# Performance work log

Measured on AMD Instinct MI355X. Metric: run time of the kernel, lower is better.

The kernel has to match this reference:

```python
import jax, jax.numpy as jnp
import numpy as np

N = 50000
E = 800000
IN_C = 128
HEADS = 2
HID = 64  # out_channels // heads (concat=True)
NEG_SLOPE = 0.2


def setup_inputs() -> dict:
    key = jax.random.key(0)
    ks = jax.random.split(key, 8)
    x = jax.random.normal(ks[0], (N, IN_C), dtype=jnp.float32)
    edge_index = jax.random.randint(ks[1], (2, E), 0, N, dtype=jnp.int64)
    edge_weight = jax.random.uniform(ks[2], (E,), dtype=jnp.float32)
    s = 1.0 / np.sqrt(IN_C)
    W_l = jax.random.normal(ks[3], (IN_C, HEADS * HID), dtype=jnp.float32) * s
    b_l = jnp.zeros((HEADS * HID,), dtype=jnp.float32)
    W_r = jax.random.normal(ks[4], (IN_C, HEADS * HID), dtype=jnp.float32) * s
    b_r = jnp.zeros((HEADS * HID,), dtype=jnp.float32)
    att = jax.random.normal(ks[5], (HEADS, HID), dtype=jnp.float32) * (1.0 / np.sqrt(HID))
    bias = jnp.zeros((HEADS * HID,), dtype=jnp.float32)
    return {"x": x, "edge_index": edge_index, "edge_weight": edge_weight,
            "W_l": W_l, "b_l": b_l, "W_r": W_r, "b_r": b_r,
            "att": att, "bias": bias}


def reference(x, edge_index, edge_weight, W_l, b_l, W_r, b_r, att, bias):
    src = edge_index[0]  # source nodes j (messages flow j -> i)
    dst = edge_index[1]  # destination nodes i
    # per-head linear transforms: [N, H, C]
    x_l = (x @ W_l + b_l).reshape(N, HEADS, HID)
    x_r = (x @ W_r + b_r).reshape(N, HEADS, HID)
    # GATv2 edge score: att . LeakyReLU(x_l[j] + x_r[i])  -> [E, H]
    e = x_l[src] + x_r[dst]
    e = jnp.where(e >= 0, e, NEG_SLOPE * e)
    alpha = jnp.einsum('ehc,hc->eh', e, att)
    # segment softmax over incoming edges of each destination node
    amax = jax.ops.segment_max(alpha, dst, num_segments=N)  # [N, H]
    alpha = jnp.exp(alpha - amax[dst])
    denom = jax.ops.segment_sum(alpha, dst, num_segments=N)  # [N, H]
    alpha = alpha / (denom[dst] + 1e-16)
    # scatter-add aggregation of weighted source features
    out = jax.ops.segment_sum(x_l[src] * alpha[:, :, None], dst, num_segments=N)
    out = out.reshape(N, HEADS * HID) + bias
    return jnp.tanh(out)
```

## Files before the change

### kernel.cpp

```cpp
#include <hip/hip_runtime.h>
#include <hip/hip_fp16.h>
#include <math.h>

#define N_NODES 50000
#define E_EDGES 800000
#define IN_CH   128
#define OUT_CH  128
#define HID     64
#define NEG_SLOPE 0.2f
#define NBLK_SCAN ((N_NODES + 255) / 256)
#define XS_STRIDE 136

typedef _Float16 half8 __attribute__((ext_vector_type(8)));
typedef _Float16 h2 __attribute__((ext_vector_type(2)));
typedef float f32x2 __attribute__((ext_vector_type(2)));
typedef float f32x4 __attribute__((ext_vector_type(4)));

template<int CTRL>
__device__ __forceinline__ float dpp_add(float a) {
    int t = __builtin_amdgcn_update_dpp(0, __float_as_int(a), CTRL, 0xF, 0xF, true);
    return a + __int_as_float(t);
}
#define REDUCE16(a)                                                          \
    a = dpp_add<0x128>(a); a = dpp_add<0x124>(a);                            \
    a = dpp_add<0x122>(a); a = dpp_add<0x121>(a);


__global__ void count_kernel(const int* __restrict__ ei, int* __restrict__ counts,
                             int* __restrict__ rank) {
    int t = blockIdx.x * blockDim.x + threadIdx.x;
    if (t * 2 < E_EDGES) {
        int2 d = *(const int2*)(ei + E_EDGES + t * 2);
        int2 r;
        r.x = atomicAdd(&counts[d.x], 1);
        r.y = atomicAdd(&counts[d.y], 1);
        *(int2*)(rank + t * 2) = r;
    }
}

__global__ __launch_bounds__(256) void scan1_kernel(const int* __restrict__ counts,
                                                    int* __restrict__ off,
                                                    int* __restrict__ tops) {
    __shared__ int s[256];
    int i = blockIdx.x * 256 + threadIdx.x;
    int v = (i < N_NODES) ? counts[i] : 0;
    s[threadIdx.x] = v;
    __syncthreads();
    for (int dlt = 1; dlt < 256; dlt <<= 1) {
        int t = (threadIdx.x >= dlt) ? s[threadIdx.x - dlt] : 0;
        __syncthreads();
        s[threadIdx.x] += t;
        __syncthreads();
    }
    if (i < N_NODES) off[i] = s[threadIdx.x] - v;
    if (threadIdx.x == 255) tops[blockIdx.x] = s[255];
}

__global__ __launch_bounds__(256) void scan2_kernel(int* __restrict__ tops) {
    __shared__ int s[256];
    int v = (threadIdx.x < NBLK_SCAN) ? tops[threadIdx.x] : 0;
    s[threadIdx.x] = v;
    __syncthreads();
    for (int dlt = 1; dlt < 256; dlt <<= 1) {
        int t = (threadIdx.x >= dlt) ? s[threadIdx.x - dlt] : 0;
        __syncthreads();
        s[threadIdx.x] += t;
        __syncthreads();
    }
    if (threadIdx.x < NBLK_SCAN) tops[threadIdx.x] = s[threadIdx.x] - v;
}

__global__ void scatter_kernel(const int* __restrict__ ei, const int* __restrict__ off,
                               const int* __restrict__ tops, const int* __restrict__ rank,
                               int* __restrict__ ssrc) {
    int t = blockIdx.x * blockDim.x + threadIdx.x;
    if (t * 2 >= E_EDGES) return;
    int2 d = *(const int2*)(ei + E_EDGES + t * 2);
    int2 s = *(const int2*)(ei + t * 2);
    int2 r = *(const int2*)(rank + t * 2);
    ssrc[tops[d.x >> 8] + off[d.x] + r.x] = s.x;
    ssrc[tops[d.y >> 8] + off[d.y] + r.y] = s.y;
}

__global__ __launch_bounds__(256) void convW_kernel(
    const float* __restrict__ Wl, const float* __restrict__ bl,
    const float* __restrict__ Wr, const float* __restrict__ br,
    __half* __restrict__ wfrag, float* __restrict__ bcat,
    int* __restrict__ counts) {
    const int gid = blockIdx.x * 256 + threadIdx.x;
    if (gid < N_NODES) counts[gid] = 0;
    if (gid >= 4096) return;
    const int n = gid & 255;
    const int c = gid >> 8;
    const int t = n >> 4, q16 = n & 15, s = c >> 2, kg = c & 3;
    const int k0 = c * 8;
    const float* __restrict__ Wsrc = (n < 128) ? Wl : Wr;
    const int col = n & 127;
    half8 h;
    #pragma unroll
    for (int j = 0; j < 8; ++j) h[j] = (_Float16)Wsrc[(k0 + j) * 128 + col];
    ((half8*)wfrag)[((t * 4 + s) * 4 + kg) * 16 + q16] = h;
    if (c == 0) bcat[n] = (n < 128) ? bl[col] : br[col];
}

__global__ __launch_bounds__(256) void linear_mfma_kernel(
    const float* __restrict__ x, const __half* __restrict__ wfrag,
    const float* __restrict__ bcat,
    __half* __restrict__ xl16, float* __restrict__ xr) {
    __shared__ __align__(16) __half xs[64 * XS_STRIDE];
    const int tid  = threadIdx.x;
    const int lane = tid & 63;
    const int wv   = tid >> 6;
    const int nodeBase = blockIdx.x * 64;

    {
        const float4* __restrict__ x4 = (const float4*)(x + (size_t)nodeBase * IN_CH);
        #pragma unroll
        for (int i = 0; i < 8; ++i) {
            const int idx = tid + i * 256;
            const int row = idx >> 5;
            const int c   = (idx & 31) * 4;
            float4 v = {0.0f, 0.0f, 0.0f, 0.0f};
            if (nodeBase + row < N_NODES) v = x4[idx];
            __half2 h01 = __floats2half2_rn(v.x, v.y);
            __half2 h23 = __floats2half2_rn(v.z, v.w);
            uint2 pk;
            pk.x = *(unsigned int*)&h01;
            pk.y = *(unsigned int*)&h23;
            *(uint2*)&xs[row * XS_STRIDE + c] = pk;
        }
    }
    __syncthreads();

    const int q16 = lane & 15;
    const int kg  = lane >> 4;

    const half8* __restrict__ wf8 = (const half8*)wfrag;
    half8 b[4][4];
    #pragma unroll
    for (int t = 0; t < 4; ++t)
        #pragma unroll
        for (int s = 0; s < 4; ++s)
            b[t][s] = wf8[(((wv * 4 + t) * 4 + s) * 4 + kg) * 16 + q16];

    #pragma unroll
    for (int m = 0; m < 4; ++m) {
        f32x4 acc[4];
        #pragma unroll
        for (int t = 0; t < 4; ++t) acc[t] = (f32x4){0.0f, 0.0f, 0.0f, 0.0f};
        #pragma unroll
        for (int s = 0; s < 4; ++s) {
            const half8 a = *(const half8*)&xs[(m * 16 + q16) * XS_STRIDE + s * 32 + kg * 8];
            #pragma unroll
            for (int t = 0; t < 4; ++t)
                acc[t] = __builtin_amdgcn_mfma_f32_16x16x32_f16(a, b[t][s], acc[t], 0, 0, 0);
        }
        const int nodeRow0 = nodeBase + m * 16 + kg * 4;
        #pragma unroll
        for (int t = 0; t < 4; ++t) {
            const int col = wv * 64 + t * 16 + q16;
            const float bv = bcat[col];
            #pragma unroll
            for (int r = 0; r < 4; ++r) {
                const int node = nodeRow0 + r;
                if (node < N_NODES) {
                    const float v = acc[t][r] + bv;
                    if (col < 128) xl16[(size_t)node * 128 + col] = __float2half_rn(v);
                    else           xr[(size_t)node * 128 + (col - 128)] = v;
                }
            }
        }
    }
}

__global__ __launch_bounds__(256) void node_agg_kernel(
    const __half* __restrict__ xl16, const float* __restrict__ xr,
    const float* __restrict__ att,
    const int* __restrict__ off, const int* __restrict__ counts,
    const int* __restrict__ tops, const int* __restrict__ ssrc,
    const float* __restrict__ bias, float* __restrict__ out) {
    const int node = (blockIdx.x * blockDim.x + threadIdx.x) >> 6;
    const int lane = threadIdx.x & 63;
    if (node >= N_NODES) return;
    const int half = lane >> 5;
    const int cl   = lane & 31;

    const uint2* __restrict__ xlh = (const uint2*)xl16;
    const float4 xrv  = ((const float4*)xr)[node * 32 + cl];
    const float4 attv = ((const float4*)att)[cl];
    const h2 xr01  = {(_Float16)xrv.x, (_Float16)xrv.y};
    const h2 xr23  = {(_Float16)xrv.z, (_Float16)xrv.w};
    const h2 att01 = {(_Float16)attv.x, (_Float16)attv.y};
    const h2 att23 = {(_Float16)attv.z, (_Float16)attv.w};
    const h2 ns2   = {(_Float16)NEG_SLOPE, (_Float16)NEG_SLOPE};

    const int cnt = counts[node];
    const int o   = tops[node >> 8] + off[node];

    float d = 0.0f;
    float4 acc = {0.0f, 0.0f, 0.0f, 0.0f};

#define SCOREH(raw, aout)                                                    \
    {                                                                        \
        h2 v01 = *(h2*)&raw.x;                                               \
        h2 v23 = *(h2*)&raw.y;                                               \
        h2 s01 = v01 + xr01;                                                 \
        h2 s23 = v23 + xr23;                                                 \
        h2 l01 = __builtin_elementwise_max(s01, s01 * ns2);                  \
        h2 l23 = __builtin_elementwise_max(s23, s23 * ns2);                  \
        aout = __builtin_amdgcn_fdot2(l01, att01,                            \
               __builtin_amdgcn_fdot2(l23, att23, 0.0f, false), false);      \
    }
#define ACCUM(raw, wgt)                                                      \
    {                                                                        \
        f32x2 f01 = __builtin_convertvector(*(h2*)&raw.x, f32x2);            \
        f32x2 f23 = __builtin_convertvector(*(h2*)&raw.y, f32x2);            \
        d += wgt;                                                            \
        acc.x = fmaf(wgt, f01.x, acc.x);                                     \
        acc.y = fmaf(wgt, f01.y, acc.y);                                     \
        acc.z = fmaf(wgt, f23.x, acc.z);                                     \
        acc.w = fmaf(wgt, f23.y, acc.w);                                     \
    }

    int k = 0;
    for (; k + 4 <= cnt; k += 4) {
        const int sA = ssrc[o + k + half];
        const int sB = ssrc[o + k + 2 + half];
        const uint2 rA = xlh[sA * 32 + cl];
        const uint2 rB = xlh[sB * 32 + cl];
        float a0, a1;
        SCOREH(rA, a0);
        SCOREH(rB, a1);
        REDUCE16(a0);
        REDUCE16(a1);
        const float eA = __expf(a0);
        const float eB = __expf(a1);
        ACCUM(rA, eA);
        ACCUM(rB, eB);
    }
    for (; k < cnt; k += 2) {
        const int eidx = k + half;
        const bool valid = (eidx < cnt);
        const int src = ssrc[o + (valid ? eidx : 0)];
        const uint2 raw = xlh[src * 32 + cl];
        float a;
        SCOREH(raw, a);
        REDUCE16(a);
        const float ev = valid ? __expf(a) : 0.0f;
        ACCUM(raw, ev);
    }
#undef SCOREH
#undef ACCUM
    acc.x += __shfl_xor(acc.x, 32);
    acc.y += __shfl_xor(acc.y, 32);
    acc.z += __shfl_xor(acc.z, 32);
    acc.w += __shfl_xor(acc.w, 32);
    d     += __shfl_xor(d, 32);

    if (lane < 32) {
        const float4 bv = ((const float4*)bias)[cl];
        const float inv = 1.0f / (d + 1e-16f);
        float4 r;
        float t;
        t = __expf(2.0f * fmaf(acc.x, inv, bv.x)); r.x = (t - 1.0f) / (t + 1.0f);
        t = __expf(2.0f * fmaf(acc.y, inv, bv.y)); r.y = (t - 1.0f) / (t + 1.0f);
        t = __expf(2.0f * fmaf(acc.z, inv, bv.z)); r.z = (t - 1.0f) / (t + 1.0f);
        t = __expf(2.0f * fmaf(acc.w, inv, bv.w)); r.w = (t - 1.0f) / (t + 1.0f);
        ((float4*)out)[node * 32 + cl] = r;
    }
}

extern "C" void kernel_launch(void* const* d_in, const int* in_sizes, int n_in,
                              void* d_out, int out_size, void* d_ws, size_t ws_size,
                              hipStream_t stream) {
    const float* x    = (const float*)d_in[0];
    const int*   ei   = (const int*)d_in[1];
    const float* Wl   = (const float*)d_in[3];
    const float* bl   = (const float*)d_in[4];
    const float* Wr   = (const float*)d_in[5];
    const float* br   = (const float*)d_in[6];
    const float* att  = (const float*)d_in[7];
    const float* bias = (const float*)d_in[8];
    float* out = (float*)d_out;

    char* ws = (char*)d_ws;
    __half* xl16  = (__half*)ws;  ws += (size_t)N_NODES * OUT_CH * 2;
    float*  xr    = (float*)ws;   ws += (size_t)N_NODES * OUT_CH * 4;
    __half* wfrag = (__half*)ws;  ws += (size_t)256 * 128 * 2;
    float*  bcat  = (float*)ws;   ws += 256 * 4;
    int*   counts = (int*)ws;     ws += (size_t)N_NODES * 4;
    int*   off    = (int*)ws;     ws += (size_t)N_NODES * 4;
    int*   tops   = (int*)ws;     ws += 256 * 4;
    int*   rank   = (int*)ws;     ws += (size_t)E_EDGES * 4;
    int*   ssrc   = (int*)ws;     ws += (size_t)E_EDGES * 4;

    const int pairBlocks = (E_EDGES / 2 + 255) / 256;

    convW_kernel<<<NBLK_SCAN, 256, 0, stream>>>(Wl, bl, Wr, br, wfrag, bcat, counts);
    linear_mfma_kernel<<<(N_NODES + 63) / 64, 256, 0, stream>>>(x, wfrag, bcat, xl16, xr);
    count_kernel<<<pairBlocks, 256, 0, stream>>>(ei, counts, rank);
    scan1_kernel<<<NBLK_SCAN, 256, 0, stream>>>(counts, off, tops);
    scan2_kernel<<<1, 256, 0, stream>>>(tops);
    scatter_kernel<<<pairBlocks, 256, 0, stream>>>(ei, off, tops, rank, ssrc);
    node_agg_kernel<<<(N_NODES + 3) / 4, 256, 0, stream>>>(
        xl16, xr, att, off, counts, tops, ssrc, bias, out);
}
```

Baseline: 124.5 us.

## Use persistent grid-stride waves and 8-edge unrolled gather in node aggregation

Node aggregation now launches a fixed grid of 2048 blocks, and each wave loops over nodes with a grid stride instead of taking a single node. The edge loop gains an 8-edges-per-iteration path, with each half-wave handling four consecutive edges, so more independent gathers are in flight. This is meant to raise memory-level parallelism and cut wave launch overhead. In exchange it uses more registers, may lower occupancy, and can balance load less evenly across the fixed grid.

```diff
diff --git a/kernel.cpp b/kernel.cpp
--- a/kernel.cpp
+++ b/kernel.cpp
@@ -179,26 +179,18 @@
     const int* __restrict__ off, const int* __restrict__ counts,
     const int* __restrict__ tops, const int* __restrict__ ssrc,
     const float* __restrict__ bias, float* __restrict__ out) {
-    const int node = (blockIdx.x * blockDim.x + threadIdx.x) >> 6;
     const int lane = threadIdx.x & 63;
-    if (node >= N_NODES) return;
     const int half = lane >> 5;
     const int cl   = lane & 31;
+    const int wid    = (blockIdx.x * blockDim.x + threadIdx.x) >> 6;
+    const int nwaves = (gridDim.x * blockDim.x) >> 6;
 
     const uint2* __restrict__ xlh = (const uint2*)xl16;
-    const float4 xrv  = ((const float4*)xr)[node * 32 + cl];
     const float4 attv = ((const float4*)att)[cl];
-    const h2 xr01  = {(_Float16)xrv.x, (_Float16)xrv.y};
-    const h2 xr23  = {(_Float16)xrv.z, (_Float16)xrv.w};
     const h2 att01 = {(_Float16)attv.x, (_Float16)attv.y};
     const h2 att23 = {(_Float16)attv.z, (_Float16)attv.w};
     const h2 ns2   = {(_Float16)NEG_SLOPE, (_Float16)NEG_SLOPE};
-
-    const int cnt = counts[node];
-    const int o   = tops[node >> 8] + off[node];
-
-    float d = 0.0f;
-    float4 acc = {0.0f, 0.0f, 0.0f, 0.0f};
+    const float4 bv = ((const float4*)bias)[cl];
 
 #define SCOREH(raw, aout)                                                    \
     {                                                                        \
@@ -222,52 +214,91 @@
         acc.w = fmaf(wgt, f23.y, acc.w);                                     \
     }
 
-    int k = 0;
-    for (; k + 4 <= cnt; k += 4) {
-        const int sA = ssrc[o + k + half];
-        const int sB = ssrc[o + k + 2 + half];
-        const uint2 rA = xlh[sA * 32 + cl];
-        const uint2 rB = xlh[sB * 32 + cl];
-        float a0, a1;
-        SCOREH(rA, a0);
-        SCOREH(rB, a1);
-        REDUCE16(a0);
-        REDUCE16(a1);
-        const float eA = __expf(a0);
-        const float eB = __expf(a1);
-        ACCUM(rA, eA);
-        ACCUM(rB, eB);
-    }
-    for (; k < cnt; k += 2) {
-        const int eidx = k + half;
-        const bool valid = (eidx < cnt);
-        const int src = ssrc[o + (valid ? eidx : 0)];
-        const uint2 raw = xlh[src * 32 + cl];
-        float a;
-        SCOREH(raw, a);
-        REDUCE16(a);
-        const float ev = valid ? __expf(a) : 0.0f;
-        ACCUM(raw, ev);
+    for (int node = wid; node < N_NODES; node += nwaves) {
+        const float4 xrv = ((const float4*)xr)[node * 32 + cl];
+        const h2 xr01 = {(_Float16)xrv.x, (_Float16)xrv.y};
+        const h2 xr23 = {(_Float16)xrv.z, (_Float16)xrv.w};
+
+        const int cnt = counts[node];
+        const int o   = tops[node >> 8] + off[node];
+
+        float d = 0.0f;
+        float4 acc = {0.0f, 0.0f, 0.0f, 0.0f};
+
+        int k = 0;
+        for (; k + 8 <= cnt; k += 8) {
+            const int base = o + k + 4 * half;
+            const int sA = ssrc[base + 0];
+            const int sB = ssrc[base + 1];
+            const int sC = ssrc[base + 2];
+            const int sD = ssrc[base + 3];
+            const uint2 rA = xlh[sA * 32 + cl];
+            const uint2 rB = xlh[sB * 32 + cl];
+            const uint2 rC = xlh[sC * 32 + cl];
+            const uint2 rD = xlh[sD * 32 + cl];
+            float a0, a1, a2, a3;
+            SCOREH(rA, a0);
+            SCOREH(rB, a1);
+            SCOREH(rC, a2);
+            SCOREH(rD, a3);
+            REDUCE16(a0);
+            REDUCE16(a1);
+            REDUCE16(a2);
+            REDUCE16(a3);
+            const float eA = __expf(a0);
+            const float eB = __expf(a1);
+            const float eC = __expf(a2);
+            const float eD = __expf(a3);
+            ACCUM(rA, eA);
+            ACCUM(rB, eB);
+            ACCUM(rC, eC);
+            ACCUM(rD, eD);
+        }
+        for (; k + 4 <= cnt; k += 4) {
+            const int sA = ssrc[o + k + half];
+            const int sB = ssrc[o + k + 2 + half];
+            const uint2 rA = xlh[sA * 32 + cl];
+            const uint2 rB = xlh[sB * 32 + cl];
+            float a0, a1;
+            SCOREH(rA, a0);
+            SCOREH(rB, a1);
+            REDUCE16(a0);
+            REDUCE16(a1);
+            const float eA = __expf(a0);
+            const float eB = __expf(a1);
+            ACCUM(rA, eA);
+            ACCUM(rB, eB);
+        }
+        for (; k < cnt; k += 2) {
+            const int eidx = k + half;
+            const bool valid = (eidx < cnt);
+            const int src = ssrc[o + (valid ? eidx : 0)];
+            const uint2 raw = xlh[src * 32 + cl];
+            float a;
+            SCOREH(raw, a);
+            REDUCE16(a);
+            const float ev = valid ? __expf(a) : 0.0f;
+            ACCUM(raw, ev);
+        }
+        acc.x += __shfl_xor(acc.x, 32);
+        acc.y += __shfl_xor(acc.y, 32);
+        acc.z += __shfl_xor(acc.z, 32);
+        acc.w += __shfl_xor(acc.w, 32);
+        d     += __shfl_xor(d, 32);
+
+        if (lane < 32) {
+            const float inv = 1.0f / (d + 1e-16f);
+            float4 r;
+            float t;
+            t = __expf(2.0f * fmaf(acc.x, inv, bv.x)); r.x = (t - 1.0f) / (t + 1.0f);
+            t = __expf(2.0f * fmaf(acc.y, inv, bv.y)); r.y = (t - 1.0f) / (t + 1.0f);
+            t = __expf(2.0f * fmaf(acc.z, inv, bv.z)); r.z = (t - 1.0f) / (t + 1.0f);
+            t = __expf(2.0f * fmaf(acc.w, inv, bv.w)); r.w = (t - 1.0f) / (t + 1.0f);
+            ((float4*)out)[node * 32 + cl] = r;
+        }
     }
 #undef SCOREH
 #undef ACCUM
-    acc.x += __shfl_xor(acc.x, 32);
-    acc.y += __shfl_xor(acc.y, 32);
-    acc.z += __shfl_xor(acc.z, 32);
-    acc.w += __shfl_xor(acc.w, 32);
-    d     += __shfl_xor(d, 32);
-
-    if (lane < 32) {
-        const float4 bv = ((const float4*)bias)[cl];
-        const float inv = 1.0f / (d + 1e-16f);
-        float4 r;
-        float t;
-        t = __expf(2.0f * fmaf(acc.x, inv, bv.x)); r.x = (t - 1.0f) / (t + 1.0f);
-        t = __expf(2.0f * fmaf(acc.y, inv, bv.y)); r.y = (t - 1.0f) / (t + 1.0f);
-        t = __expf(2.0f * fmaf(acc.z, inv, bv.z)); r.z = (t - 1.0f) / (t + 1.0f);
-        t = __expf(2.0f * fmaf(acc.w, inv, bv.w)); r.w = (t - 1.0f) / (t + 1.0f);
-        ((float4*)out)[node * 32 + cl] = r;
-    }
 }
 
 extern "C" void kernel_launch(void* const* d_in, const int* in_sizes, int n_in,
@@ -302,6 +333,6 @@
     scan1_kernel<<<NBLK_SCAN, 256, 0, stream>>>(counts, off, tops);
     scan2_kernel<<<1, 256, 0, stream>>>(tops);
     scatter_kernel<<<pairBlocks, 256, 0, stream>>>(ei, off, tops, rank, ssrc);
-    node_agg_kernel<<<(N_NODES + 3) / 4, 256, 0, stream>>>(
+    node_agg_kernel<<<2048, 256, 0, stream>>>(
         xl16, xr, att, off, counts, tops, ssrc, bias, out);
 }
```

Result: no change. 123.0 us (-1.2%).

## Fuse degree count into linear kernel and merge scan passes via last-block ticket

Applied to the files above, without the earlier changes.

Moves the per-edge destination degree counting (atomics and rank output) into the tail of the MFMA linear kernel as a grid-stride loop. The second-level scan of block totals now runs inside scan1, performed by the last block to finish, which it detects with an atomic ticket counter reset in convW. The scatter kernel now handles four edges per thread with int4 loads. Together these cut two kernel launches and overlap the atomic counting with the GEMM. The cost is a longer tail in the linear kernel, plus reliance on atomic visibility to make the last-block pattern correct.

```diff
diff --git a/kernel.cpp b/kernel.cpp
--- a/kernel.cpp
+++ b/kernel.cpp
@@ -25,70 +25,14 @@
     a = dpp_add<0x128>(a); a = dpp_add<0x124>(a);                            \
     a = dpp_add<0x122>(a); a = dpp_add<0x121>(a);
 
-
-__global__ void count_kernel(const int* __restrict__ ei, int* __restrict__ counts,
-                             int* __restrict__ rank) {
-    int t = blockIdx.x * blockDim.x + threadIdx.x;
-    if (t * 2 < E_EDGES) {
-        int2 d = *(const int2*)(ei + E_EDGES + t * 2);
-        int2 r;
-        r.x = atomicAdd(&counts[d.x], 1);
-        r.y = atomicAdd(&counts[d.y], 1);
-        *(int2*)(rank + t * 2) = r;
-    }
-}
-
-__global__ __launch_bounds__(256) void scan1_kernel(const int* __restrict__ counts,
-                                                    int* __restrict__ off,
-                                                    int* __restrict__ tops) {
-    __shared__ int s[256];
-    int i = blockIdx.x * 256 + threadIdx.x;
-    int v = (i < N_NODES) ? counts[i] : 0;
-    s[threadIdx.x] = v;
-    __syncthreads();
-    for (int dlt = 1; dlt < 256; dlt <<= 1) {
-        int t = (threadIdx.x >= dlt) ? s[threadIdx.x - dlt] : 0;
-        __syncthreads();
-        s[threadIdx.x] += t;
-        __syncthreads();
-    }
-    if (i < N_NODES) off[i] = s[threadIdx.x] - v;
-    if (threadIdx.x == 255) tops[blockIdx.x] = s[255];
-}
-
-__global__ __launch_bounds__(256) void scan2_kernel(int* __restrict__ tops) {
-    __shared__ int s[256];
-    int v = (threadIdx.x < NBLK_SCAN) ? tops[threadIdx.x] : 0;
-    s[threadIdx.x] = v;
-    __syncthreads();
-    for (int dlt = 1; dlt < 256; dlt <<= 1) {
-        int t = (threadIdx.x >= dlt) ? s[threadIdx.x - dlt] : 0;
-        __syncthreads();
-        s[threadIdx.x] += t;
-        __syncthreads();
-    }
-    if (threadIdx.x < NBLK_SCAN) tops[threadIdx.x] = s[threadIdx.x] - v;
-}
-
-__global__ void scatter_kernel(const int* __restrict__ ei, const int* __restrict__ off,
-                               const int* __restrict__ tops, const int* __restrict__ rank,
-                               int* __restrict__ ssrc) {
-    int t = blockIdx.x * blockDim.x + threadIdx.x;
-    if (t * 2 >= E_EDGES) return;
-    int2 d = *(const int2*)(ei + E_EDGES + t * 2);
-    int2 s = *(const int2*)(ei + t * 2);
-    int2 r = *(const int2*)(rank + t * 2);
-    ssrc[tops[d.x >> 8] + off[d.x] + r.x] = s.x;
-    ssrc[tops[d.y >> 8] + off[d.y] + r.y] = s.y;
-}
-
 __global__ __launch_bounds__(256) void convW_kernel(
     const float* __restrict__ Wl, const float* __restrict__ bl,
     const float* __restrict__ Wr, const float* __restrict__ br,
     __half* __restrict__ wfrag, float* __restrict__ bcat,
-    int* __restrict__ counts) {
+    int* __restrict__ counts, int* __restrict__ done) {
     const int gid = blockIdx.x * 256 + threadIdx.x;
     if (gid < N_NODES) counts[gid] = 0;
+    if (gid == 0) *done = 0;
     if (gid >= 4096) return;
     const int n = gid & 255;
     const int c = gid >> 8;
@@ -106,7 +50,8 @@
 __global__ __launch_bounds__(256) void linear_mfma_kernel(
     const float* __restrict__ x, const __half* __restrict__ wfrag,
     const float* __restrict__ bcat,
-    __half* __restrict__ xl16, float* __restrict__ xr) {
+    __half* __restrict__ xl16, float* __restrict__ xr,
+    const int* __restrict__ ei, int* __restrict__ counts, int* __restrict__ rank) {
     __shared__ __align__(16) __half xs[64 * XS_STRIDE];
     const int tid  = threadIdx.x;
     const int lane = tid & 63;
@@ -171,6 +116,66 @@
             }
         }
     }
+
+    const int gtid = blockIdx.x * 256 + tid;
+    const int nthr = gridDim.x * 256;
+    for (int p = gtid; p * 2 < E_EDGES; p += nthr) {
+        int2 dd = *(const int2*)(ei + E_EDGES + p * 2);
+        int2 rr;
+        rr.x = atomicAdd(&counts[dd.x], 1);
+        rr.y = atomicAdd(&counts[dd.y], 1);
+        *(int2*)(rank + p * 2) = rr;
+    }
+}
+
+__global__ __launch_bounds__(256) void scan1_kernel(const int* __restrict__ counts,
+                                                    int* __restrict__ off,
+                                                    int* __restrict__ tops,
+                                                    int* __restrict__ done) {
+    __shared__ int s[256];
+    __shared__ int ticket;
+    int i = blockIdx.x * 256 + threadIdx.x;
+    int v = (i < N_NODES) ? counts[i] : 0;
+    s[threadIdx.x] = v;
+    __syncthreads();
+    for (int dlt = 1; dlt < 256; dlt <<= 1) {
+        int t = (threadIdx.x >= dlt) ? s[threadIdx.x - dlt] : 0;
+        __syncthreads();
+        s[threadIdx.x] += t;
+        __syncthreads();
+    }
+    if (i < N_NODES) off[i] = s[threadIdx.x] - v;
+    if (threadIdx.x == 255) {
+        atomicExch(&tops[blockIdx.x], s[255]);
+        ticket = atomicAdd(done, 1);
+    }
+    __syncthreads();
+    if (ticket == NBLK_SCAN - 1) {
+        int tv = (threadIdx.x < NBLK_SCAN) ? atomicAdd(&tops[threadIdx.x], 0) : 0;
+        s[threadIdx.x] = tv;
+        __syncthreads();
+        for (int dlt = 1; dlt < 256; dlt <<= 1) {
+            int t = (threadIdx.x >= dlt) ? s[threadIdx.x - dlt] : 0;
+            __syncthreads();
+            s[threadIdx.x] += t;
+            __syncthreads();
+        }
+        if (threadIdx.x < NBLK_SCAN) atomicExch(&tops[threadIdx.x], s[threadIdx.x] - tv);
+    }
+}
+
+__global__ void scatter_kernel(const int* __restrict__ ei, const int* __restrict__ off,
+                               const int* __restrict__ tops, const int* __restrict__ rank,
+                               int* __restrict__ ssrc) {
+    int t = blockIdx.x * blockDim.x + threadIdx.x;
+    if (t * 4 >= E_EDGES) return;
+    int4 d = *(const int4*)(ei + E_EDGES + t * 4);
+    int4 s = *(const int4*)(ei + t * 4);
+    int4 r = *(const int4*)(rank + t * 4);
+    ssrc[tops[d.x >> 8] + off[d.x] + r.x] = s.x;
+    ssrc[tops[d.y >> 8] + off[d.y] + r.y] = s.y;
+    ssrc[tops[d.z >> 8] + off[d.z] + r.z] = s.z;
+    ssrc[tops[d.w >> 8] + off[d.w] + r.w] = s.w;
 }
 
 __global__ __launch_bounds__(256) void node_agg_kernel(
@@ -291,17 +296,15 @@
     int*   counts = (int*)ws;     ws += (size_t)N_NODES * 4;
     int*   off    = (int*)ws;     ws += (size_t)N_NODES * 4;
     int*   tops   = (int*)ws;     ws += 256 * 4;
+    int*   done   = (int*)ws;     ws += 16;
     int*   rank   = (int*)ws;     ws += (size_t)E_EDGES * 4;
     int*   ssrc   = (int*)ws;     ws += (size_t)E_EDGES * 4;
 
-    const int pairBlocks = (E_EDGES / 2 + 255) / 256;
-
-    convW_kernel<<<NBLK_SCAN, 256, 0, stream>>>(Wl, bl, Wr, br, wfrag, bcat, counts);
-    linear_mfma_kernel<<<(N_NODES + 63) / 64, 256, 0, stream>>>(x, wfrag, bcat, xl16, xr);
-    count_kernel<<<pairBlocks, 256, 0, stream>>>(ei, counts, rank);
-    scan1_kernel<<<NBLK_SCAN, 256, 0, stream>>>(counts, off, tops);
-    scan2_kernel<<<1, 256, 0, stream>>>(tops);
-    scatter_kernel<<<pairBlocks, 256, 0, stream>>>(ei, off, tops, rank, ssrc);
+    convW_kernel<<<NBLK_SCAN, 256, 0, stream>>>(Wl, bl, Wr, br, wfrag, bcat, counts, done);
+    linear_mfma_kernel<<<(N_NODES + 63) / 64, 256, 0, stream>>>(
+        x, wfrag, bcat, xl16, xr, ei, counts, rank);
+    scan1_kernel<<<NBLK_SCAN, 256, 0, stream>>>(counts, off, tops, done);
+    scatter_kernel<<<(E_EDGES / 4 + 255) / 256, 256, 0, stream>>>(ei, off, tops, rank, ssrc);
     node_agg_kernel<<<(N_NODES + 3) / 4, 256, 0, stream>>>(
         xl16, xr, att, off, counts, tops, ssrc, bias, out);
 }
```

Result: slower. 134.6 us (+8.1%).
